# Kernel optimization log

Measured on AMD Instinct MI355X. Metric: run time of the kernel, lower is better.

Reference implementation:

```python
import jax, jax.numpy as jnp
import numpy as np

HIDDEN = 4096
NUM_HEADS = 32
NUM_KV_HEADS = 8
HEAD_DIM = 128
ROPE_THETA = 10000.0


def setup_inputs() -> dict:
    key = jax.random.key(0)
    ks = jax.random.split(key, 5)
    B, N = 2, 2048
    s = 0.02
    return {
        "hidden_states": jax.random.normal(ks[0], (B, N, HIDDEN), dtype=jnp.float32),
        "positions": jnp.tile(jnp.arange(N, dtype=jnp.int32)[None, :], (B, 1)),
        "Wq": jax.random.normal(ks[1], (HIDDEN, NUM_HEADS * HEAD_DIM), dtype=jnp.float32) * s,
        "Wk": jax.random.normal(ks[2], (HIDDEN, NUM_KV_HEADS * HEAD_DIM), dtype=jnp.float32) * s,
        "Wv": jax.random.normal(ks[3], (HIDDEN, NUM_KV_HEADS * HEAD_DIM), dtype=jnp.float32) * s,
        "Wo": jax.random.normal(ks[4], (NUM_HEADS * HEAD_DIM, HIDDEN), dtype=jnp.float32) * s,
    }


def _rotate_half(x):
    half = x.shape[-1] // 2
    return jnp.concatenate([-x[..., half:], x[..., :half]], axis=-1)


def reference(hidden_states, positions, Wq, Wk, Wv, Wo):
    B, N, _ = hidden_states.shape
    H, KVH, D = NUM_HEADS, NUM_KV_HEADS, HEAD_DIM
    rep = H // KVH

    # projections
    q = (hidden_states @ Wq).reshape(B, N, H, D).transpose(0, 2, 1, 3)     # [B,H,N,D]
    k = (hidden_states @ Wk).reshape(B, N, KVH, D).transpose(0, 2, 1, 3)   # [B,KVH,N,D]
    v = (hidden_states @ Wv).reshape(B, N, KVH, D).transpose(0, 2, 1, 3)   # [B,KVH,N,D]

    # rotary embedding
    inv_freq = 1.0 / (ROPE_THETA ** (jnp.arange(0, D, 2, dtype=jnp.float32) / D))
    freqs = positions.astype(jnp.float32)[..., None] * inv_freq            # [B,N,D/2]
    emb = jnp.concatenate([freqs, freqs], axis=-1)                          # [B,N,D]
    cos = jnp.cos(emb)[:, None, :, :]                                       # [B,1,N,D]
    sin = jnp.sin(emb)[:, None, :, :]
    q = q * cos + _rotate_half(q) * sin
    k = k * cos + _rotate_half(k) * sin

    # GQA attention without materializing repeated k/v:
    # group q heads by kv head (repeat_interleave => q head h uses kv group h//rep)
    qg = q.reshape(B, KVH, rep, N, D)
    scale = 1.0 / jnp.sqrt(jnp.asarray(D, dtype=q.dtype))
    scores = jnp.einsum('bgrnd,bgmd->bgrnm', qg, k) * scale                 # [B,KVH,rep,N,N]
    causal = jnp.tril(jnp.ones((N, N), dtype=bool))
    scores = jnp.where(causal, scores, jnp.finfo(scores.dtype).min)
    attn = jax.nn.softmax(scores, axis=-1)
    out = jnp.einsum('bgrnm,bgmd->bgrnd', attn, v)                          # [B,KVH,rep,N,D]
    out = out.reshape(B, H, N, D).transpose(0, 2, 1, 3).reshape(B, N, H * D)
    return out @ Wo
```

## Files before the change

kernel.cpp:

```cpp
#include <hip/hip_runtime.h>
#include <hip/hip_bf16.h>

typedef __bf16 bf16_t;
typedef float  f32x4  __attribute__((ext_vector_type(4)));
typedef bf16_t bf16x4 __attribute__((ext_vector_type(4)));
typedef bf16_t bf16x8 __attribute__((ext_vector_type(8)));

#define MFMA16(a, b, c) __builtin_amdgcn_mfma_f32_16x16x32_bf16((a), (b), (c), 0, 0, 0)

#define GLOAD_LDS16(g, l)                                                              \
  __builtin_amdgcn_global_load_lds((const __attribute__((address_space(1))) void*)(g), \
                                   (__attribute__((address_space(3))) void*)(l), 16, 0, 0)

#define BARRIER    __builtin_amdgcn_s_barrier()
#define WAIT_LGKM0 asm volatile("s_waitcnt lgkmcnt(0)" ::: "memory")
#define WAIT_LGKM8 asm volatile("s_waitcnt lgkmcnt(8)" ::: "memory")
#define WAIT_VM4   asm volatile("s_waitcnt vmcnt(4)" ::: "memory")
#define WAIT_VM0   asm volatile("s_waitcnt vmcnt(0)" ::: "memory")

__global__ __launch_bounds__(256) void cvt_bf16(const float* __restrict__ in,
                                                bf16_t* __restrict__ out, int n4) {
  int stride = gridDim.x * blockDim.x;
  for (int i = blockIdx.x * blockDim.x + threadIdx.x; i < n4; i += stride) {
    f32x4 v = ((const f32x4*)in)[i];
    bf16x4 o;
#pragma unroll
    for (int j = 0; j < 4; ++j) o[j] = (bf16_t)v[j];
    ((bf16x4*)out)[i] = o;
  }
}

__global__ __launch_bounds__(256) void transpose_cvt(const float* __restrict__ in,
                                                     bf16_t* __restrict__ out,
                                                     int R, int C) {
  __shared__ float t[64][65];
  int tr0 = blockIdx.y * 64, tc0 = blockIdx.x * 64;
  int tx = threadIdx.x & 15, ty = threadIdx.x >> 4;
#pragma unroll
  for (int i = 0; i < 4; ++i) {
    f32x4 v = *(const f32x4*)(in + (size_t)(tr0 + ty + 16 * i) * C + tc0 + tx * 4);
#pragma unroll
    for (int j = 0; j < 4; ++j) t[ty + 16 * i][tx * 4 + j] = v[j];
  }
  __syncthreads();
#pragma unroll
  for (int i = 0; i < 4; ++i) {
    bf16x4 o4;
#pragma unroll
    for (int j = 0; j < 4; ++j) o4[j] = (bf16_t)t[tx * 4 + j][ty + 16 * i];
    *(bf16x4*)(out + (size_t)(tc0 + ty + 16 * i) * R + tr0 + tx * 4) = o4;
  }
}

#define LDB8(bf)                                                                         \
  {                                                                                      \
    const int sb_ = bBase0 + (bf)*16384;                                                 \
    _Pragma("unroll") for (int nf = 0; nf < 4; ++nf) {                                   \
      int row_ = brow0 + nf * 16 + ci;                                                   \
      _Pragma("unroll") for (int ks = 0; ks < 2; ++ks)                                   \
          b[nf][ks] = *(const bf16x8*)&lds[sb_ + row_ * 64 + ((ks * 32 + g * 8) ^ co)];  \
    }                                                                                    \
  }

#define LDA4(bf, q)                                                                      \
  {                                                                                      \
    const int sb_ = aBase0 + (bf)*16384;                                                 \
    _Pragma("unroll") for (int j = 0; j < 2; ++j) {                                      \
      int row_ = ((q)*2 + j) * 16 + ci;                                                  \
      _Pragma("unroll") for (int ks = 0; ks < 2; ++ks)                                   \
          a[j][ks] = *(const bf16x8*)&lds[sb_ + row_ * 64 + ((ks * 32 + g * 8) ^ co)];   \
    }                                                                                    \
  }

#define MMQ(q)                                                                           \
  {                                                                                      \
    __builtin_amdgcn_s_setprio(1);                                                       \
    _Pragma("unroll") for (int j = 0; j < 2; ++j)                                        \
        _Pragma("unroll") for (int nf = 0; nf < 4; ++nf)                                 \
            _Pragma("unroll") for (int ks = 0; ks < 2; ++ks)                             \
                acc[(q)*2 + j][nf] = MFMA16(a[j][ks], b[nf][ks], acc[(q)*2 + j][nf]);    \
    __builtin_amdgcn_s_setprio(0);                                                       \
  }

template <int WRITE_BF16>
__global__ __launch_bounds__(512) void gemm8(const bf16_t* __restrict__ A,
                                             const bf16_t* __restrict__ Bt,
                                             void* __restrict__ Cv,
                                             int N, int K, int ntn) {
  __shared__ alignas(16) bf16_t lds[65536];
  const int tid = threadIdx.x;
  const int lane = tid & 63, w = tid >> 6;
  const int wr = w >> 2, wc = w & 3;
  const int g = lane >> 4, ci = lane & 15;
  const int cpx = gridDim.x >> 3;
  const int wg = ((int)blockIdx.x & 7) * cpx + ((int)blockIdx.x >> 3);
  const int m0 = (wg / ntn) * 256, n0 = (wg % ntn) * 256;
  const int ksw = ((lane & 7) ^ (lane >> 3)) << 3;
  const int aBase0 = wr * 8192;
  const int bBase0 = 32768 + (wc >> 1) * 8192;
  const int brow0 = (wc & 1) * 64;
  const int co = (ci & 7) << 3;

  const bf16_t* As[2] = {A + (size_t)m0 * K, A + (size_t)(m0 + 128) * K};
  const bf16_t* Bs[2] = {Bt + (size_t)n0 * K, Bt + (size_t)(n0 + 128) * K};

  auto stage = [&](const bf16_t* src, int kk, int ldsbase) {
#pragma unroll
    for (int j = 0; j < 2; ++j)
      GLOAD_LDS16(src + (size_t)(j * 64 + w * 8 + (lane >> 3)) * K + kk + ksw,
                  (char*)&lds[ldsbase + (j * 64 + w * 8) * 64]);
  };

  bf16x8 a[2][2], b[4][2];
  f32x4 acc[8][4];
#pragma unroll
  for (int mf = 0; mf < 8; ++mf)
#pragma unroll
    for (int nf = 0; nf < 4; ++nf) acc[mf][nf] = f32x4{0.f, 0.f, 0.f, 0.f};

  stage(As[0], 0, 0);
  stage(As[1], 0, 8192);
  stage(Bs[0], 0, 32768);
  stage(Bs[1], 0, 40960);
  stage(Bs[0], 64, 49152);
  stage(Bs[1], 64, 57344);
  WAIT_VM4;
  BARRIER;

  const int NT2 = K >> 7;
  for (int i = 0; i < NT2; ++i) {
    const int keb = i << 7;
    const int kA1 = keb + 64;
    int e2 = keb + 128;
    if (e2 > K - 64) e2 = K - 64;
    int o2 = keb + 192;
    if (o2 > K - 64) o2 = K - 64;
    LDA4(0, 0) LDB8(0)
    stage(As[0], kA1, 16384);
    WAIT_LGKM8;
    BARRIER; WAIT_LGKM0;
    MMQ(0)
    BARRIER;
    LDA4(0, 1)
    stage(As[1], kA1, 24576);
    BARRIER; WAIT_LGKM0;
    MMQ(1)
    BARRIER;
    LDA4(0, 2)
    stage(Bs[0], e2, 32768);
    BARRIER; WAIT_LGKM0;
    MMQ(2)
    BARRIER;
    LDA4(0, 3)
    stage(Bs[1], e2, 40960);
    BARRIER; WAIT_LGKM0;
    MMQ(3)
    WAIT_VM4;
    BARRIER;
    LDA4(1, 0) LDB8(1)
    stage(As[0], e2, 0);
    WAIT_LGKM8;
    BARRIER; WAIT_LGKM0;
    MMQ(0)
    BARRIER;
    LDA4(1, 1)
    stage(As[1], e2, 8192);
    BARRIER; WAIT_LGKM0;
    MMQ(1)
    BARRIER;
    LDA4(1, 2)
    stage(Bs[0], o2, 49152);
    BARRIER; WAIT_LGKM0;
    MMQ(2)
    BARRIER;
    LDA4(1, 3)
    stage(Bs[1], o2, 57344);
    BARRIER; WAIT_LGKM0;
    MMQ(3)
    WAIT_VM4;
    BARRIER;
  }
  WAIT_VM0;

#pragma unroll
  for (int mf = 0; mf < 8; ++mf) {
#pragma unroll
    for (int nf = 0; nf < 4; ++nf) {
      int grow = m0 + wr * 128 + mf * 16 + g * 4;
      int gcol = n0 + wc * 64 + nf * 16 + ci;
#pragma unroll
      for (int r = 0; r < 4; ++r) {
        if (WRITE_BF16)
          ((bf16_t*)Cv)[(size_t)(grow + r) * N + gcol] = (bf16_t)acc[mf][nf][r];
        else
          ((float*)Cv)[(size_t)(grow + r) * N + gcol] = acc[mf][nf][r];
      }
    }
  }
}

__global__ __launch_bounds__(256) void rope_pack(const bf16_t* __restrict__ QKV,
                                                 const int* __restrict__ pos,
                                                 bf16_t* __restrict__ Qr,
                                                 bf16_t* __restrict__ Kr,
                                                 bf16_t* __restrict__ Vr) {
  int unit = blockIdx.x * 4 + (threadIdx.x >> 6);
  int lane = threadIdx.x & 63;
  int token = unit / 48, slot = unit % 48;
  int b = token >> 11, n = token & 2047;
  const bf16_t* base = QKV + (size_t)token * 6144;
  if (slot < 40) {
    float p = (float)pos[token];
    float inv = exp2f(-(float)lane * 0.20762050593045702f);
    float ang = p * inv;
    float sn, cs;
    sincosf(ang, &sn, &cs);
    const bf16_t* src;
    bf16_t* dst;
    if (slot < 32) {
      src = base + slot * 128;
      dst = Qr + ((size_t)(b * 32 + slot) * 2048 + n) * 128;
    } else {
      int kvh = slot - 32;
      src = base + 4096 + kvh * 128;
      dst = Kr + ((size_t)(b * 8 + kvh) * 2048 + n) * 128;
    }
    float x0 = (float)src[lane], x1 = (float)src[lane + 64];
    dst[lane] = (bf16_t)(x0 * cs - x1 * sn);
    dst[lane + 64] = (bf16_t)(x1 * cs + x0 * sn);
  } else {
    int kvh = slot - 40;
    const bf16_t* src = base + 5120 + kvh * 128;
    bf16_t* dst = Vr + ((size_t)(b * 8 + kvh) * 2048 + n) * 128;
    dst[lane] = src[lane];
    dst[lane + 64] = src[lane + 64];
  }
}

__global__ __launch_bounds__(512) void attn_kernel(const bf16_t* __restrict__ Q,
                                                   const bf16_t* __restrict__ K,
                                                   const bf16_t* __restrict__ V,
                                                   bf16_t* __restrict__ O) {
  const float scale = 0.08838834764831845f;
  __shared__ alignas(16) bf16_t Kl[64 * 128];
  __shared__ alignas(16) bf16_t Vt[128 * 64];
  __shared__ alignas(16) bf16_t Pl[8][32 * 64];
  const int tid = threadIdx.x;
  const int lane = tid & 63, w = tid >> 6;
  const int g = lane >> 4, ci = lane & 15;
  const int hb = blockIdx.y;
  const int b = hb >> 5, h = hb & 31, kvh = h >> 2;
  const int p = blockIdx.x;
  const int qtB = 15 - p;
  const int qr[2] = {p * 128 + w * 16, qtB * 128 + w * 16};
  const bf16_t* Qh = Q + (size_t)hb * 2048 * 128;
  const bf16_t* Kh = K + (size_t)(b * 8 + kvh) * 2048 * 128;
  const bf16_t* Vh = V + (size_t)(b * 8 + kvh) * 2048 * 128;

  bf16x8 bq[2][4];
#pragma unroll
  for (int qb = 0; qb < 2; ++qb)
#pragma unroll
    for (int ks = 0; ks < 4; ++ks)
      bq[qb][ks] = *(const bf16x8*)(Qh + (size_t)(qr[qb] + ci) * 128 + ks * 32 + g * 8);

  f32x4 o[2][8];
#pragma unroll
  for (int qb = 0; qb < 2; ++qb)
#pragma unroll
    for (int nb = 0; nb < 8; ++nb) o[qb][nb] = f32x4{0.f, 0.f, 0.f, 0.f};
  float mrow[2] = {-1e30f, -1e30f};
  float lrow[2] = {0.f, 0.f};

  const int nt = (qtB + 1) * 2;
  for (int t = 0; t < nt; ++t) {
    const int kv0 = t * 64;
    __syncthreads();
#pragma unroll
    for (int i = 0; i < 2; ++i) {
      int c = tid + i * 512;
      int row = c >> 4, kc = (c & 15) * 8;
      bf16x8 kx = *(const bf16x8*)(Kh + (size_t)(kv0 + row) * 128 + kc);
      int sw = ((row ^ (row >> 3)) & 7) << 4;
      *(bf16x8*)((char*)Kl + row * 256 + ((kc * 2) ^ sw)) = kx;
    }
    {
      int kq = tid >> 5, dq = tid & 31;
      bf16x4 rv[4];
#pragma unroll
      for (int rr = 0; rr < 4; ++rr)
        rv[rr] = *(const bf16x4*)(Vh + (size_t)(kv0 + kq * 4 + rr) * 128 + dq * 4);
#pragma unroll
      for (int jj = 0; jj < 4; ++jj) {
        int d = dq * 4 + jj;
        bf16x4 cv;
#pragma unroll
        for (int rr = 0; rr < 4; ++rr) cv[rr] = rv[rr][jj];
        int sw = ((d ^ (d >> 3)) & 7) << 4;
        *(bf16x4*)((char*)Vt + d * 128 + ((kq * 8) ^ sw)) = cv;
      }
    }
    __syncthreads();

    bool act[2] = {kv0 <= qr[0] + 15, kv0 <= qr[1] + 15};
#pragma unroll
    for (int qb = 0; qb < 2; ++qb) {
      if (!act[qb]) continue;
      f32x4 st[4];
#pragma unroll
      for (int kvb = 0; kvb < 4; ++kvb) st[kvb] = f32x4{0.f, 0.f, 0.f, 0.f};
      __builtin_amdgcn_s_setprio(1);
#pragma unroll
      for (int kvb = 0; kvb < 4; ++kvb) {
        int row = kvb * 16 + ci;
        int sw = ((row ^ (row >> 3)) & 7) << 4;
#pragma unroll
        for (int ks = 0; ks < 4; ++ks) {
          bf16x8 ak = *(const bf16x8*)((char*)Kl + row * 256 + ((ks * 64 + g * 16) ^ sw));
          st[kvb] = MFMA16(ak, bq[qb][ks], st[kvb]);
        }
      }
      __builtin_amdgcn_s_setprio(0);
      const int q = qr[qb] + ci;
      const bool needmask = (kv0 + 63 > qr[qb]);
      float pv[16];
      float pm = -1e30f;
#pragma unroll
      for (int kvb = 0; kvb < 4; ++kvb)
#pragma unroll
        for (int r = 0; r < 4; ++r) {
          float v = st[kvb][r] * scale;
          if (needmask && (kv0 + kvb * 16 + 4 * g + r > q)) v = -1e30f;
          pv[kvb * 4 + r] = v;
          pm = fmaxf(pm, v);
        }
      pm = fmaxf(pm, __shfl_xor(pm, 16));
      pm = fmaxf(pm, __shfl_xor(pm, 32));
      const bool nskip = !__all((int)(pm <= mrow[qb] + 8.0f));
      const float mold = mrow[qb];
      float mnew = mold;
      float fs = 1.0f;
      if (nskip) {
        mnew = fmaxf(mold, pm);
        fs = __expf(mold - mnew);
        mrow[qb] = mnew;
      }
      float ps = 0.f;
#pragma unroll
      for (int e = 0; e < 16; ++e) {
        pv[e] = __expf(pv[e] - mnew);
        ps += pv[e];
      }
      ps += __shfl_xor(ps, 16);
      ps += __shfl_xor(ps, 32);
      lrow[qb] = (nskip ? lrow[qb] * fs : lrow[qb]) + ps;
      int prow = qb * 16 + ci;
      int swp = ((prow ^ (prow >> 3)) & 7) << 4;
#pragma unroll
      for (int kvb = 0; kvb < 4; ++kvb) {
        bf16x4 pk;
#pragma unroll
        for (int r = 0; r < 4; ++r) pk[r] = (bf16_t)pv[kvb * 4 + r];
        *(bf16x4*)((char*)&Pl[w][0] + prow * 128 + (((kvb * 16 + 4 * g) * 2) ^ swp)) = pk;
      }
      if (nskip) {
        float fo[4];
#pragma unroll
        for (int r = 0; r < 4; ++r) fo[r] = __shfl(fs, 4 * g + r);
#pragma unroll
        for (int nb = 0; nb < 8; ++nb)
#pragma unroll
          for (int r = 0; r < 4; ++r) o[qb][nb][r] *= fo[r];
      }
    }
    bf16x8 pa[2][2];
#pragma unroll
    for (int qb = 0; qb < 2; ++qb) {
      if (!act[qb]) continue;
      int prow = qb * 16 + ci;
      int swp = ((prow ^ (prow >> 3)) & 7) << 4;
#pragma unroll
      for (int ks = 0; ks < 2; ++ks)
        pa[qb][ks] = *(const bf16x8*)((char*)&Pl[w][0] + prow * 128 + ((ks * 64 + g * 16) ^ swp));
    }
    __builtin_amdgcn_s_setprio(1);
#pragma unroll
    for (int nb = 0; nb < 8; ++nb) {
      int d = nb * 16 + ci;
      int sw = ((d ^ (d >> 3)) & 7) << 4;
      bf16x8 bv0 = *(const bf16x8*)((char*)Vt + d * 128 + ((g * 16) ^ sw));
      bf16x8 bv1 = *(const bf16x8*)((char*)Vt + d * 128 + ((64 + g * 16) ^ sw));
#pragma unroll
      for (int qb = 0; qb < 2; ++qb) {
        if (!act[qb]) continue;
        o[qb][nb] = MFMA16(pa[qb][0], bv0, o[qb][nb]);
        o[qb][nb] = MFMA16(pa[qb][1], bv1, o[qb][nb]);
      }
    }
    __builtin_amdgcn_s_setprio(0);
  }
#pragma unroll
  for (int qb = 0; qb < 2; ++qb) {
    float linv = 1.0f / lrow[qb];
    float lv[4];
#pragma unroll
    for (int r = 0; r < 4; ++r) lv[r] = __shfl(linv, 4 * g + r);
#pragma unroll
    for (int r = 0; r < 4; ++r) {
      int n = qr[qb] + 4 * g + r;
      bf16_t* op = O + (size_t)(b * 2048 + n) * 4096 + h * 128;
#pragma unroll
      for (int nb = 0; nb < 8; ++nb) op[nb * 16 + ci] = (bf16_t)(o[qb][nb][r] * lv[r]);
    }
  }
}

extern "C" void kernel_launch(void* const* d_in, const int* in_sizes, int n_in,
                              void* d_out, int out_size, void* d_ws, size_t ws_size,
                              hipStream_t stream) {
  (void)in_sizes; (void)n_in; (void)out_size; (void)ws_size;
  const float* X = (const float*)d_in[0];
  const int* pos = (const int*)d_in[1];
  const float* Wq = (const float*)d_in[2];
  const float* Wk = (const float*)d_in[3];
  const float* Wv = (const float*)d_in[4];
  const float* Wo = (const float*)d_in[5];
  float* out = (float*)d_out;

  char* w = (char*)d_ws;
  auto carve = [&](size_t bytes) {
    void* p = (void*)w;
    w += (bytes + 255) & ~(size_t)255;
    return p;
  };
  const size_t T = 4096;
  bf16_t* Xbf    = (bf16_t*)carve(T * 4096 * 2);
  bf16_t* WqkvT  = (bf16_t*)carve(6144ull * 4096 * 2);
  bf16_t* WoT    = (bf16_t*)carve(4096ull * 4096 * 2);
  bf16_t* QKVraw = (bf16_t*)carve(T * 6144 * 2);
  bf16_t* Qr     = (bf16_t*)carve(T * 4096 * 2);
  bf16_t* Kr     = (bf16_t*)carve(T * 1024 * 2);
  bf16_t* Vr     = (bf16_t*)carve(T * 1024 * 2);
  bf16_t* Obf    = (bf16_t*)carve(T * 4096 * 2);

  cvt_bf16<<<2048, 256, 0, stream>>>(X, Xbf, (int)(T * 4096 / 4));
  transpose_cvt<<<dim3(64, 64), 256, 0, stream>>>(Wq, WqkvT, 4096, 4096);
  transpose_cvt<<<dim3(16, 64), 256, 0, stream>>>(Wk, WqkvT + 4096ull * 4096, 4096, 1024);
  transpose_cvt<<<dim3(16, 64), 256, 0, stream>>>(Wv, WqkvT + 5120ull * 4096, 4096, 1024);
  transpose_cvt<<<dim3(64, 64), 256, 0, stream>>>(Wo, WoT, 4096, 4096);

  gemm8<1><<<384, 512, 0, stream>>>(Xbf, WqkvT, QKVraw, 6144, 4096, 24);

  rope_pack<<<(int)(T * 48 / 4), 256, 0, stream>>>(QKVraw, pos, Qr, Kr, Vr);

  attn_kernel<<<dim3(8, 64), 512, 0, stream>>>(Qr, Kr, Vr, Obf);

  gemm8<0><<<256, 512, 0, stream>>>(Obf, WoT, out, 4096, 4096, 16);
}
```

Before: 582.8 us.

## Switch GEMM to 32x32 MFMA tiles and prefetch attention K/V into registers

The GEMM inner loop now uses 32x32x16 bf16 MFMA with 16-wide accumulators instead of 16x16x32, which halves the number of LDS fragment reads per MFMA and changes the output write mapping. Separately, the attention kernel loads the next K/V tile from global memory into registers while the current tile is being computed, so global latency overlaps with MFMA work. The costs are a different LDS read pattern that may introduce bank conflicts under the existing swizzle, plus higher register pressure in both kernels.

```diff
diff --git a/kernel.cpp b/kernel.cpp
--- a/kernel.cpp
+++ b/kernel.cpp
@@ -2,11 +2,13 @@
 #include <hip/hip_bf16.h>
 
 typedef __bf16 bf16_t;
-typedef float  f32x4  __attribute__((ext_vector_type(4)));
-typedef bf16_t bf16x4 __attribute__((ext_vector_type(4)));
-typedef bf16_t bf16x8 __attribute__((ext_vector_type(8)));
+typedef float  f32x4   __attribute__((ext_vector_type(4)));
+typedef float  f32x16  __attribute__((ext_vector_type(16)));
+typedef bf16_t bf16x4  __attribute__((ext_vector_type(4)));
+typedef bf16_t bf16x8  __attribute__((ext_vector_type(8)));
 
 #define MFMA16(a, b, c) __builtin_amdgcn_mfma_f32_16x16x32_bf16((a), (b), (c), 0, 0, 0)
+#define MFMA32(a, b, c) __builtin_amdgcn_mfma_f32_32x32x16_bf16((a), (b), (c), 0, 0, 0)
 
 #define GLOAD_LDS16(g, l)                                                              \
   __builtin_amdgcn_global_load_lds((const __attribute__((address_space(1))) void*)(g), \
@@ -55,30 +57,27 @@
 #define LDB8(bf)                                                                         \
   {                                                                                      \
     const int sb_ = bBase0 + (bf)*16384;                                                 \
-    _Pragma("unroll") for (int nf = 0; nf < 4; ++nf) {                                   \
-      int row_ = brow0 + nf * 16 + ci;                                                   \
-      _Pragma("unroll") for (int ks = 0; ks < 2; ++ks)                                   \
-          b[nf][ks] = *(const bf16x8*)&lds[sb_ + row_ * 64 + ((ks * 32 + g * 8) ^ co)];  \
+    _Pragma("unroll") for (int nf = 0; nf < 2; ++nf) {                                   \
+      int row_ = brow0 + nf * 32 + li31;                                                 \
+      _Pragma("unroll") for (int ks = 0; ks < 4; ++ks)                                   \
+          b[nf][ks] = *(const bf16x8*)&lds[sb_ + row_ * 64 + ((ks * 16 + hi8) ^ co)];    \
     }                                                                                    \
   }
 
 #define LDA4(bf, q)                                                                      \
   {                                                                                      \
     const int sb_ = aBase0 + (bf)*16384;                                                 \
-    _Pragma("unroll") for (int j = 0; j < 2; ++j) {                                      \
-      int row_ = ((q)*2 + j) * 16 + ci;                                                  \
-      _Pragma("unroll") for (int ks = 0; ks < 2; ++ks)                                   \
-          a[j][ks] = *(const bf16x8*)&lds[sb_ + row_ * 64 + ((ks * 32 + g * 8) ^ co)];   \
-    }                                                                                    \
+    const int row_ = (q)*32 + li31;                                                      \
+    _Pragma("unroll") for (int ks = 0; ks < 4; ++ks)                                     \
+        a[ks] = *(const bf16x8*)&lds[sb_ + row_ * 64 + ((ks * 16 + hi8) ^ co)];          \
   }
 
 #define MMQ(q)                                                                           \
   {                                                                                      \
     __builtin_amdgcn_s_setprio(1);                                                       \
-    _Pragma("unroll") for (int j = 0; j < 2; ++j)                                        \
-        _Pragma("unroll") for (int nf = 0; nf < 4; ++nf)                                 \
-            _Pragma("unroll") for (int ks = 0; ks < 2; ++ks)                             \
-                acc[(q)*2 + j][nf] = MFMA16(a[j][ks], b[nf][ks], acc[(q)*2 + j][nf]);    \
+    _Pragma("unroll") for (int nf = 0; nf < 2; ++nf)                                     \
+        _Pragma("unroll") for (int ks = 0; ks < 4; ++ks)                                 \
+            acc[q][nf] = MFMA32(a[ks], b[nf][ks], acc[q][nf]);                           \
     __builtin_amdgcn_s_setprio(0);                                                       \
   }
 
@@ -91,7 +90,7 @@
   const int tid = threadIdx.x;
   const int lane = tid & 63, w = tid >> 6;
   const int wr = w >> 2, wc = w & 3;
-  const int g = lane >> 4, ci = lane & 15;
+  const int li31 = lane & 31, hi8 = (lane >> 5) * 8;
   const int cpx = gridDim.x >> 3;
   const int wg = ((int)blockIdx.x & 7) * cpx + ((int)blockIdx.x >> 3);
   const int m0 = (wg / ntn) * 256, n0 = (wg % ntn) * 256;
@@ -99,7 +98,7 @@
   const int aBase0 = wr * 8192;
   const int bBase0 = 32768 + (wc >> 1) * 8192;
   const int brow0 = (wc & 1) * 64;
-  const int co = (ci & 7) << 3;
+  const int co = (lane & 7) << 3;
 
   const bf16_t* As[2] = {A + (size_t)m0 * K, A + (size_t)(m0 + 128) * K};
   const bf16_t* Bs[2] = {Bt + (size_t)n0 * K, Bt + (size_t)(n0 + 128) * K};
@@ -111,12 +110,14 @@
                   (char*)&lds[ldsbase + (j * 64 + w * 8) * 64]);
   };
 
-  bf16x8 a[2][2], b[4][2];
-  f32x4 acc[8][4];
-#pragma unroll
-  for (int mf = 0; mf < 8; ++mf)
-#pragma unroll
-    for (int nf = 0; nf < 4; ++nf) acc[mf][nf] = f32x4{0.f, 0.f, 0.f, 0.f};
+  bf16x8 a[4], b[2][4];
+  f32x16 acc[4][2];
+#pragma unroll
+  for (int mf = 0; mf < 4; ++mf)
+#pragma unroll
+    for (int nf = 0; nf < 2; ++nf)
+#pragma unroll
+      for (int e = 0; e < 16; ++e) acc[mf][nf][e] = 0.f;
 
   stage(As[0], 0, 0);
   stage(As[1], 0, 8192);
@@ -183,17 +184,17 @@
   WAIT_VM0;
 
 #pragma unroll
-  for (int mf = 0; mf < 8; ++mf) {
-#pragma unroll
-    for (int nf = 0; nf < 4; ++nf) {
-      int grow = m0 + wr * 128 + mf * 16 + g * 4;
-      int gcol = n0 + wc * 64 + nf * 16 + ci;
-#pragma unroll
-      for (int r = 0; r < 4; ++r) {
+  for (int mf = 0; mf < 4; ++mf) {
+#pragma unroll
+    for (int nf = 0; nf < 2; ++nf) {
+      int gcol = n0 + wc * 64 + nf * 32 + li31;
+#pragma unroll
+      for (int r = 0; r < 16; ++r) {
+        int grow = m0 + wr * 128 + mf * 32 + (r & 3) + 8 * (r >> 2) + (hi8 >> 1);
         if (WRITE_BF16)
-          ((bf16_t*)Cv)[(size_t)(grow + r) * N + gcol] = (bf16_t)acc[mf][nf][r];
+          ((bf16_t*)Cv)[(size_t)grow * N + gcol] = (bf16_t)acc[mf][nf][r];
         else
-          ((float*)Cv)[(size_t)(grow + r) * N + gcol] = acc[mf][nf][r];
+          ((float*)Cv)[(size_t)grow * N + gcol] = acc[mf][nf][r];
       }
     }
   }
@@ -272,35 +273,46 @@
   float mrow[2] = {-1e30f, -1e30f};
   float lrow[2] = {0.f, 0.f};
 
+  bf16x8 kreg[2];
+  bf16x4 rv[4];
+  const int kq = tid >> 5, dq = tid & 31;
+  auto loadKV = [&](int kv0) {
+#pragma unroll
+    for (int i = 0; i < 2; ++i) {
+      int c = tid + i * 512;
+      kreg[i] = *(const bf16x8*)(Kh + (size_t)(kv0 + (c >> 4)) * 128 + (c & 15) * 8);
+    }
+#pragma unroll
+    for (int rr = 0; rr < 4; ++rr)
+      rv[rr] = *(const bf16x4*)(Vh + (size_t)(kv0 + kq * 4 + rr) * 128 + dq * 4);
+  };
+  auto writeKV = [&]() {
+#pragma unroll
+    for (int i = 0; i < 2; ++i) {
+      int c = tid + i * 512;
+      int row = c >> 4, kc = (c & 15) * 8;
+      int sw = ((row ^ (row >> 3)) & 7) << 4;
+      *(bf16x8*)((char*)Kl + row * 256 + ((kc * 2) ^ sw)) = kreg[i];
+    }
+#pragma unroll
+    for (int jj = 0; jj < 4; ++jj) {
+      int d = dq * 4 + jj;
+      bf16x4 cv;
+#pragma unroll
+      for (int rr = 0; rr < 4; ++rr) cv[rr] = rv[rr][jj];
+      int sw = ((d ^ (d >> 3)) & 7) << 4;
+      *(bf16x4*)((char*)Vt + d * 128 + ((kq * 8) ^ sw)) = cv;
+    }
+  };
+
   const int nt = (qtB + 1) * 2;
+  loadKV(0);
   for (int t = 0; t < nt; ++t) {
     const int kv0 = t * 64;
     __syncthreads();
-#pragma unroll
-    for (int i = 0; i < 2; ++i) {
-      int c = tid + i * 512;
-      int row = c >> 4, kc = (c & 15) * 8;
-      bf16x8 kx = *(const bf16x8*)(Kh + (size_t)(kv0 + row) * 128 + kc);
-      int sw = ((row ^ (row >> 3)) & 7) << 4;
-      *(bf16x8*)((char*)Kl + row * 256 + ((kc * 2) ^ sw)) = kx;
-    }
-    {
-      int kq = tid >> 5, dq = tid & 31;
-      bf16x4 rv[4];
-#pragma unroll
-      for (int rr = 0; rr < 4; ++rr)
-        rv[rr] = *(const bf16x4*)(Vh + (size_t)(kv0 + kq * 4 + rr) * 128 + dq * 4);
-#pragma unroll
-      for (int jj = 0; jj < 4; ++jj) {
-        int d = dq * 4 + jj;
-        bf16x4 cv;
-#pragma unroll
-        for (int rr = 0; rr < 4; ++rr) cv[rr] = rv[rr][jj];
-        int sw = ((d ^ (d >> 3)) & 7) << 4;
-        *(bf16x4*)((char*)Vt + d * 128 + ((kq * 8) ^ sw)) = cv;
-      }
-    }
+    writeKV();
     __syncthreads();
+    if (t + 1 < nt) loadKV(kv0 + 64);
 
     bool act[2] = {kv0 <= qr[0] + 15, kv0 <= qr[1] + 15};
 #pragma unroll
```

Measured after the change: 607.2 us. 1.04x slower.

## Retile QKV GEMM to 256x192 tiles and prefetch K/V in attention

Applied to the files above, without the earlier changes.

Adds a dedicated QKV projection GEMM using 256x192 output tiles with 8 waves arranged 4x2, giving 512 workgroups instead of 384 so work spreads more evenly across CUs, with its own LDS staging schedule. In the attention kernel, K/V tile loads from global memory are issued into registers one iteration ahead and written to LDS at the next step, overlapping global latency with the MFMA work. The new GEMM has a different per-wave MFMA/LDS ratio and a custom waitcnt schedule. The register prefetch raises register pressure in attention.

```diff
diff --git a/kernel.cpp b/kernel.cpp
--- a/kernel.cpp
+++ b/kernel.cpp
@@ -15,6 +15,7 @@
 #define BARRIER    __builtin_amdgcn_s_barrier()
 #define WAIT_LGKM0 asm volatile("s_waitcnt lgkmcnt(0)" ::: "memory")
 #define WAIT_LGKM8 asm volatile("s_waitcnt lgkmcnt(8)" ::: "memory")
+#define WAIT_VM3   asm volatile("s_waitcnt vmcnt(3)" ::: "memory")
 #define WAIT_VM4   asm volatile("s_waitcnt vmcnt(4)" ::: "memory")
 #define WAIT_VM0   asm volatile("s_waitcnt vmcnt(0)" ::: "memory")
 
@@ -83,10 +84,10 @@
   }
 
 template <int WRITE_BF16>
-__global__ __launch_bounds__(512) void gemm8(const bf16_t* __restrict__ A,
-                                             const bf16_t* __restrict__ Bt,
-                                             void* __restrict__ Cv,
-                                             int N, int K, int ntn) {
+__global__ __launch_bounds__(512) void gemm8o(const bf16_t* __restrict__ A,
+                                              const bf16_t* __restrict__ Bt,
+                                              void* __restrict__ Cv,
+                                              int N, int K, int ntn) {
   __shared__ alignas(16) bf16_t lds[65536];
   const int tid = threadIdx.x;
   const int lane = tid & 63, w = tid >> 6;
@@ -195,6 +196,148 @@
         else
           ((float*)Cv)[(size_t)(grow + r) * N + gcol] = acc[mf][nf][r];
       }
+    }
+  }
+}
+
+#define QLDB12(bf)                                                                        \
+  {                                                                                       \
+    const int sb_ = 32768 + (bf)*12288;                                                   \
+    _Pragma("unroll") for (int nf = 0; nf < 6; ++nf) {                                    \
+      int row_ = wc * 96 + nf * 16 + ci;                                                  \
+      _Pragma("unroll") for (int ks = 0; ks < 2; ++ks)                                    \
+          b[nf][ks] = *(const bf16x8*)&lds[sb_ + row_ * 64 + ((ks * 32 + g * 8) ^ co)];   \
+    }                                                                                     \
+  }
+
+#define QLDA2(bf, q)                                                                      \
+  {                                                                                       \
+    const int sb_ = (bf)*16384;                                                           \
+    const int row_ = wr * 64 + (q)*16 + ci;                                               \
+    _Pragma("unroll") for (int ks = 0; ks < 2; ++ks)                                      \
+        a[ks] = *(const bf16x8*)&lds[sb_ + row_ * 64 + ((ks * 32 + g * 8) ^ co)];         \
+  }
+
+#define QMMQ(q)                                                                           \
+  {                                                                                       \
+    __builtin_amdgcn_s_setprio(1);                                                        \
+    _Pragma("unroll") for (int nf = 0; nf < 6; ++nf)                                      \
+        _Pragma("unroll") for (int ks = 0; ks < 2; ++ks)                                  \
+            acc[q][nf] = MFMA16(a[ks], b[nf][ks], acc[q][nf]);                            \
+    __builtin_amdgcn_s_setprio(0);                                                        \
+  }
+
+__global__ __launch_bounds__(512) void gemm8qkv(const bf16_t* __restrict__ A,
+                                                const bf16_t* __restrict__ Bt,
+                                                bf16_t* __restrict__ C,
+                                                int N, int K, int ntn) {
+  __shared__ alignas(16) bf16_t lds[57344];
+  const int tid = threadIdx.x;
+  const int lane = tid & 63, w = tid >> 6;
+  const int wr = w >> 1, wc = w & 1;
+  const int g = lane >> 4, ci = lane & 15;
+  const int cpx = gridDim.x >> 3;
+  const int wg = ((int)blockIdx.x & 7) * cpx + ((int)blockIdx.x >> 3);
+  const int m0 = (wg / ntn) * 256, n0 = (wg % ntn) * 192;
+  const int ksw = ((lane & 7) ^ (lane >> 3)) << 3;
+  const int co = (ci & 7) << 3;
+
+  const bf16_t* Ar[4] = {A + (size_t)m0 * K, A + (size_t)(m0 + 64) * K,
+                         A + (size_t)(m0 + 128) * K, A + (size_t)(m0 + 192) * K};
+  const bf16_t* Br[3] = {Bt + (size_t)n0 * K, Bt + (size_t)(n0 + 64) * K,
+                         Bt + (size_t)(n0 + 128) * K};
+
+  auto stage64 = [&](const bf16_t* src, int kk, int ldsbase) {
+    GLOAD_LDS16(src + (size_t)(w * 8 + (lane >> 3)) * K + kk + ksw,
+                (char*)&lds[ldsbase + w * 512]);
+  };
+
+  bf16x8 a[2], b[6][2];
+  f32x4 acc[4][6];
+#pragma unroll
+  for (int mf = 0; mf < 4; ++mf)
+#pragma unroll
+    for (int nf = 0; nf < 6; ++nf) acc[mf][nf] = f32x4{0.f, 0.f, 0.f, 0.f};
+
+#pragma unroll
+  for (int c = 0; c < 4; ++c) stage64(Ar[c], 0, c * 4096);
+#pragma unroll
+  for (int c = 0; c < 3; ++c) stage64(Br[c], 0, 32768 + c * 4096);
+#pragma unroll
+  for (int c = 0; c < 3; ++c) stage64(Br[c], 64, 45056 + c * 4096);
+  WAIT_VM3;
+  BARRIER;
+
+  const int NT2 = K >> 7;
+  for (int i = 0; i < NT2; ++i) {
+    const int keb = i << 7;
+    const int kA1 = keb + 64;
+    int e2 = keb + 128;
+    if (e2 > K - 64) e2 = K - 64;
+    int o2 = keb + 192;
+    if (o2 > K - 64) o2 = K - 64;
+    QLDA2(0, 0) QLDB12(0)
+    stage64(Ar[0], kA1, 16384);
+    stage64(Ar[1], kA1, 16384 + 4096);
+    WAIT_LGKM8;
+    BARRIER; WAIT_LGKM0;
+    QMMQ(0)
+    BARRIER;
+    QLDA2(0, 1)
+    stage64(Ar[2], kA1, 16384 + 8192);
+    stage64(Ar[3], kA1, 16384 + 12288);
+    BARRIER; WAIT_LGKM0;
+    QMMQ(1)
+    BARRIER;
+    QLDA2(0, 2)
+    stage64(Br[0], e2, 32768);
+    stage64(Br[1], e2, 32768 + 4096);
+    BARRIER; WAIT_LGKM0;
+    QMMQ(2)
+    BARRIER;
+    QLDA2(0, 3)
+    stage64(Br[2], e2, 32768 + 8192);
+    BARRIER; WAIT_LGKM0;
+    QMMQ(3)
+    WAIT_VM3;
+    BARRIER;
+    QLDA2(1, 0) QLDB12(1)
+    stage64(Ar[0], e2, 0);
+    stage64(Ar[1], e2, 4096);
+    WAIT_LGKM8;
+    BARRIER; WAIT_LGKM0;
+    QMMQ(0)
+    BARRIER;
+    QLDA2(1, 1)
+    stage64(Ar[2], e2, 8192);
+    stage64(Ar[3], e2, 12288);
+    BARRIER; WAIT_LGKM0;
+    QMMQ(1)
+    BARRIER;
+    QLDA2(1, 2)
+    stage64(Br[0], o2, 45056);
+    stage64(Br[1], o2, 45056 + 4096);
+    BARRIER; WAIT_LGKM0;
+    QMMQ(2)
+    BARRIER;
+    QLDA2(1, 3)
+    stage64(Br[2], o2, 45056 + 8192);
+    BARRIER; WAIT_LGKM0;
+    QMMQ(3)
+    WAIT_VM3;
+    BARRIER;
+  }
+  WAIT_VM0;
+
+#pragma unroll
+  for (int mf = 0; mf < 4; ++mf) {
+#pragma unroll
+    for (int nf = 0; nf < 6; ++nf) {
+      int grow = m0 + wr * 64 + mf * 16 + g * 4;
+      int gcol = n0 + wc * 96 + nf * 16 + ci;
+#pragma unroll
+      for (int r = 0; r < 4; ++r)
+        C[(size_t)(grow + r) * N + gcol] = (bf16_t)acc[mf][nf][r];
     }
   }
 }
@@ -272,35 +415,46 @@
   float mrow[2] = {-1e30f, -1e30f};
   float lrow[2] = {0.f, 0.f};
 
+  bf16x8 kreg[2];
+  bf16x4 rv[4];
+  const int kq = tid >> 5, dq = tid & 31;
+  auto loadKV = [&](int kv0) {
+#pragma unroll
+    for (int i = 0; i < 2; ++i) {
+      int c = tid + i * 512;
+      kreg[i] = *(const bf16x8*)(Kh + (size_t)(kv0 + (c >> 4)) * 128 + (c & 15) * 8);
+    }
+#pragma unroll
+    for (int rr = 0; rr < 4; ++rr)
+      rv[rr] = *(const bf16x4*)(Vh + (size_t)(kv0 + kq * 4 + rr) * 128 + dq * 4);
+  };
+  auto writeKV = [&]() {
+#pragma unroll
+    for (int i = 0; i < 2; ++i) {
+      int c = tid + i * 512;
+      int row = c >> 4, kc = (c & 15) * 8;
+      int sw = ((row ^ (row >> 3)) & 7) << 4;
+      *(bf16x8*)((char*)Kl + row * 256 + ((kc * 2) ^ sw)) = kreg[i];
+    }
+#pragma unroll
+    for (int jj = 0; jj < 4; ++jj) {
+      int d = dq * 4 + jj;
+      bf16x4 cv;
+#pragma unroll
+      for (int rr = 0; rr < 4; ++rr) cv[rr] = rv[rr][jj];
+      int sw = ((d ^ (d >> 3)) & 7) << 4;
+      *(bf16x4*)((char*)Vt + d * 128 + ((kq * 8) ^ sw)) = cv;
+    }
+  };
+
   const int nt = (qtB + 1) * 2;
+  loadKV(0);
   for (int t = 0; t < nt; ++t) {
     const int kv0 = t * 64;
     __syncthreads();
-#pragma unroll
-    for (int i = 0; i < 2; ++i) {
-      int c = tid + i * 512;
-      int row = c >> 4, kc = (c & 15) * 8;
-      bf16x8 kx = *(const bf16x8*)(Kh + (size_t)(kv0 + row) * 128 + kc);
-      int sw = ((row ^ (row >> 3)) & 7) << 4;
-      *(bf16x8*)((char*)Kl + row * 256 + ((kc * 2) ^ sw)) = kx;
-    }
-    {
-      int kq = tid >> 5, dq = tid & 31;
-      bf16x4 rv[4];
-#pragma unroll
-      for (int rr = 0; rr < 4; ++rr)
-        rv[rr] = *(const bf16x4*)(Vh + (size_t)(kv0 + kq * 4 + rr) * 128 + dq * 4);
-#pragma unroll
-      for (int jj = 0; jj < 4; ++jj) {
-        int d = dq * 4 + jj;
-        bf16x4 cv;
-#pragma unroll
-        for (int rr = 0; rr < 4; ++rr) cv[rr] = rv[rr][jj];
-        int sw = ((d ^ (d >> 3)) & 7) << 4;
-        *(bf16x4*)((char*)Vt + d * 128 + ((kq * 8) ^ sw)) = cv;
-      }
-    }
+    writeKV();
     __syncthreads();
+    if (t + 1 < nt) loadKV(kv0 + 64);
 
     bool act[2] = {kv0 <= qr[0] + 15, kv0 <= qr[1] + 15};
 #pragma unroll
@@ -449,11 +603,11 @@
   transpose_cvt<<<dim3(16, 64), 256, 0, stream>>>(Wv, WqkvT + 5120ull * 4096, 4096, 1024);
   transpose_cvt<<<dim3(64, 64), 256, 0, stream>>>(Wo, WoT, 4096, 4096);
 
-  gemm8<1><<<384, 512, 0, stream>>>(Xbf, WqkvT, QKVraw, 6144, 4096, 24);
+  gemm8qkv<<<512, 512, 0, stream>>>(Xbf, WqkvT, QKVraw, 6144, 4096, 32);
 
   rope_pack<<<(int)(T * 48 / 4), 256, 0, stream>>>(QKVraw, pos, Qr, Kr, Vr);
 
   attn_kernel<<<dim3(8, 64), 512, 0, stream>>>(Qr, Kr, Vr, Obf);
 
-  gemm8<0><<<256, 512, 0, stream>>>(Obf, WoT, out, 4096, 4096, 16);
+  gemm8o<0><<<256, 512, 0, stream>>>(Obf, WoT, out, 4096, 4096, 16);
 }
```

After: 540.4 us. 1.08x faster.
